# Kernel tuning notes

Measured on AMD Instinct MI355X. Metric: run time of the kernel, lower is better.

## Reference

```python
import jax, jax.numpy as jnp
import numpy as np


def setup_inputs() -> dict:
    key = jax.random.key(0)
    k1, k2 = jax.random.split(key)
    x = jax.random.normal(k1, (32, 512, 2048), dtype=jnp.float32)
    codebook = jax.random.normal(k2, (1024, 512), dtype=jnp.float32)
    return {"x": x, "codebook": codebook}


def reference(x, codebook):
    # x: [N, width, T], codebook: [nb_code, code_dim], width == code_dim
    N, width, T = x.shape
    nb_code = codebook.shape[0]
    # preprocess: [N, width, T] -> [N*T, width]
    xf = jnp.transpose(x, (0, 2, 1)).reshape(-1, width)
    dist = (jnp.sum(xf * xf, axis=-1, keepdims=True)
            - 2.0 * jnp.matmul(xf, codebook.T)
            + jnp.sum(codebook * codebook, axis=-1)[None, :])
    code_idx = jnp.argmin(dist, axis=-1)  # [N*T]
    # dequantize (embedding gather)
    x_d = codebook[code_idx]  # [N*T, width]
    # perplexity over code usage histogram
    counts = jax.ops.segment_sum(jnp.ones(code_idx.shape, dtype=x.dtype),
                                 code_idx, num_segments=nb_code)
    prob = counts / jnp.sum(counts)
    perplexity = jnp.exp(-jnp.sum(prob * jnp.log(prob + 1e-7)))
    # commitment loss against detached quantized vectors
    commit_loss = jnp.mean((xf - jax.lax.stop_gradient(x_d)) ** 2)
    # straight-through estimator
    out = xf + jax.lax.stop_gradient(x_d - xf)
    out = out.reshape(N, T, width).transpose(0, 2, 1)  # [N, width, T]
    return out, code_idx.reshape(N, T), commit_loss, perplexity
```

## Files before the change

kernel.cpp:

```cpp
#include <hip/hip_runtime.h>
#include <cstddef>
#include <cstdint>

#define N_BATCH 32
#define WIDTH   512
#define T_DIM   2048
#define NB_CODE 1024
#define M_ROWS  65536
#define OUT_ELEMS 33554432
#define IDX_OFF  OUT_ELEMS
#define LOSS_OFF (OUT_ELEMS + M_ROWS)
#define PERP_OFF (LOSS_OFF + 1)
#define MARGIN   0.75f

typedef __attribute__((ext_vector_type(8))) short vshort8;
typedef __attribute__((ext_vector_type(4))) float vfloat4;
typedef __attribute__((ext_vector_type(16))) float vfloat16;

typedef __attribute__((address_space(1))) const uint32_t gu32_t;
typedef __attribute__((address_space(3))) uint32_t lu32_t;
static __device__ __forceinline__ void gload16(const void* g, void* l) {
    __builtin_amdgcn_global_load_lds((gu32_t*)g, (lu32_t*)l, 16, 0, 0);
}

static __device__ __forceinline__ unsigned short f2bf(float f) {
    uint32_t u = __float_as_uint(f);
    uint32_t r = (u + 0x7FFFu + ((u >> 16) & 1u)) >> 16;
    return (unsigned short)r;
}


__global__ __launch_bounds__(128) void k_prep(const float* __restrict__ cb,
                                              unsigned short* __restrict__ cbh,
                                              float* __restrict__ cnorm,
                                              int* __restrict__ hist) {
    const int c = blockIdx.x, tid = threadIdx.x;
    float4 v = ((const float4*)(cb + (size_t)c * WIDTH))[tid];
    ushort4 h;
    h.x = f2bf(v.x); h.y = f2bf(v.y); h.z = f2bf(v.z); h.w = f2bf(v.w);
    ((ushort4*)(cbh + (size_t)c * WIDTH))[tid] = h;
    float s = v.x * v.x + v.y * v.y + v.z * v.z + v.w * v.w;
#pragma unroll
    for (int off = 32; off >= 1; off >>= 1) s += __shfl_xor(s, off, 64);
    __shared__ float sw[2];
    if ((tid & 63) == 0) sw[tid >> 6] = s;
    __syncthreads();
    if (tid == 0) { cnorm[c] = sw[0] + sw[1]; hist[c] = 0; }
}

__global__ __launch_bounds__(256, 2) void k_argmin(
    const float* __restrict__ x, const unsigned short* __restrict__ cbh,
    const float* __restrict__ cnorm, uint32_t* __restrict__ cand,
    float* __restrict__ sbest, float* __restrict__ xnorm) {
    __shared__ __align__(16) short lds[2][16384];

    const int tid = threadIdx.x;
    const int wv = tid >> 6, l = tid & 63;
    const int l31 = l & 31, hi = l >> 5;

    int srcoff[8];
#pragma unroll
    for (int j = 0; j < 8; ++j) {
        const int q = j * 256 + tid;
        const int code = q >> 6, w = q & 63;
        const int kb = w >> 4, s = w & 15;
        srcoff[j] = code * 1024 + kb * 256 + ((s ^ (code & 15)) << 4);
    }

#define STAGE(SP, B) do {                                                     \
    const char* cbbase_ = ((const char*)cbh) + (size_t)(SP) * 32768;          \
    short* lb_ = &lds[B][0];                                                  \
    _Pragma("unroll")                                                         \
    for (int j = 0; j < 8; ++j)                                               \
        gload16(cbbase_ + srcoff[j], lb_ + (j * 256 + tid) * 8);              \
} while (0)

    STAGE(0, 0);

    const int m0w = blockIdx.x * 128 + wv * 32;
    const int n = m0w >> 11;
    const int tcol = (m0w & 2047) + l31;
    vshort8 xh[32];
    float xn = 0.f;
    {
        const float* xb = x + (size_t)n * WIDTH * T_DIM + (size_t)hi * 8 * T_DIM + tcol;
        union U8 { uint32_t u[4]; vshort8 v; };
#pragma unroll
        for (int ks = 0; ks < 32; ++ks) {
            U8 u;
#pragma unroll
            for (int j = 0; j < 4; ++j) {
                const float f0 = xb[(size_t)(ks * 16 + 2 * j) * T_DIM];
                const float f1 = xb[(size_t)(ks * 16 + 2 * j + 1) * T_DIM];
                xn = fmaf(f0, f0, fmaf(f1, f1, xn));
                asm("v_cvt_pk_bf16_f32 %0, %1, %2" : "=v"(u.u[j]) : "v"(f0), "v"(f1));
            }
            xh[ks] = u.v;
        }
    }
    xn += __shfl_xor(xn, 32, 64);
    if (l < 32) xnorm[m0w + l] = xn;

    const int sxl = l31 & 15;
    const int rbase = l31 * 512;

    float b1 = 3.4e38f, b2 = 3.4e38f, b3 = 3.4e38f;
    int i1 = 0, i2 = 0, i3 = 0;

#define INS3(S, C) do {                                                       \
        const bool lt1 = (S) < b1, lt2 = (S) < b2, lt3 = (S) < b3;            \
        b3 = lt3 ? (lt2 ? b2 : (S)) : b3;  i3 = lt3 ? (lt2 ? i2 : (C)) : i3; \
        b2 = lt2 ? (lt1 ? b1 : (S)) : b2;  i2 = lt2 ? (lt1 ? i1 : (C)) : i2; \
        b1 = lt1 ? (S) : b1;               i1 = lt1 ? (C) : i1;              \
    } while (0)

    __syncthreads();

    for (int sp = 0; sp < 32; ++sp) {
        if (sp) {
            asm volatile("s_waitcnt vmcnt(0)" ::: "memory");
            __builtin_amdgcn_s_barrier();
        }
        if (sp < 31) {
            if (sp & 1) STAGE(sp + 1, 0); else STAGE(sp + 1, 1);
        }
        const short* buf = lds[sp & 1];
        vfloat16 acc = {};
        __builtin_amdgcn_s_setprio(1);
#pragma unroll
        for (int ks = 0; ks < 32; ++ks) {
            const int addr = rbase + (ks >> 3) * 128 +
                             (((((ks & 7) << 1) | hi) ^ sxl) << 3);
            vshort8 a = *(const vshort8*)&buf[addr];
            acc = __builtin_amdgcn_mfma_f32_32x32x16_bf16(a, xh[ks], acc, 0, 0, 0);
        }
        __builtin_amdgcn_s_setprio(0);
        const int cb0 = sp * 32;
#pragma unroll
        for (int g = 0; g < 4; ++g) {
            const int cbase = cb0 + g * 8 + 4 * hi;
            const vfloat4 cn = *(const vfloat4*)&cnorm[cbase];
#pragma unroll
            for (int j = 0; j < 4; ++j) {
                const float s = fmaf(-2.f, acc[g * 4 + j], cn[j]);
                INS3(s, cbase + j);
            }
        }
    }

    {
        const float ob1 = __shfl_xor(b1, 32, 64), ob2 = __shfl_xor(b2, 32, 64), ob3 = __shfl_xor(b3, 32, 64);
        const int oi1 = __shfl_xor(i1, 32, 64), oi2 = __shfl_xor(i2, 32, 64), oi3 = __shfl_xor(i3, 32, 64);
        INS3(ob1, oi1); INS3(ob2, oi2); INS3(ob3, oi3);
    }
    if (l < 32) {
        const uint32_t f2 = (b2 - b1 < MARGIN) ? 1u : 0u;
        const uint32_t f3 = (b3 - b1 < MARGIN) ? 1u : 0u;
        cand[m0w + l] = (uint32_t)i1 | ((uint32_t)i2 << 10) | ((uint32_t)i3 << 20) | (f2 << 30) | (f3 << 31);
        sbest[m0w + l] = b1;
    }
}

__global__ __launch_bounds__(256) void k_tail(
    const float* __restrict__ x, const float* __restrict__ cb,
    const float* __restrict__ cnorm, const uint32_t* __restrict__ cand,
    const float* __restrict__ sbest, const float* __restrict__ xnorm,
    float* __restrict__ dout, int* __restrict__ hist,
    float* __restrict__ lossPart) {
    __shared__ int sidx[64];
    __shared__ float sls[64];
    __shared__ int list[64];
    __shared__ int cnt;
    __shared__ float tile[64][130];
    const int tid = threadIdx.x;
    const int b = blockIdx.x;
    const int m0 = b * 64;
    if (tid == 0) cnt = 0;
    __syncthreads();
    if (tid < 64) {
        const uint32_t wv = cand[m0 + tid];
        sidx[tid] = (int)(wv & 1023u);
        sls[tid] = xnorm[m0 + tid] + sbest[m0 + tid];
        if (wv >> 30) { const int p = atomicAdd(&cnt, 1); list[p] = tid; }
    }
    __syncthreads();
    const int nf = cnt;
    const int w = tid >> 6, lid = tid & 63;
    for (int it = w; it < nf; it += 4) {
        const int row = m0 + list[it];
        const uint32_t wv = cand[row];
        const int j1 = (int)(wv & 1023u), j2 = (int)((wv >> 10) & 1023u), j3 = (int)((wv >> 20) & 1023u);
        const bool nd3 = (wv >> 31) & 1u;
        const int n = row >> 11, t = row & 2047;
        const float* xc = x + (size_t)n * WIDTH * T_DIM + t;
        float xv[8];
#pragma unroll
        for (int e = 0; e < 8; ++e)
            xv[e] = xc[(size_t)(lid * 8 + e) * T_DIM];
        float d1 = 0.f, d2 = 0.f, d3 = 0.f;
        {
            const float* c1 = cb + (size_t)j1 * WIDTH + lid * 8;
            const float* c2 = cb + (size_t)j2 * WIDTH + lid * 8;
            const float* c3 = cb + (size_t)j3 * WIDTH + lid * 8;
            float4 a0 = *(const float4*)c1, a1 = *(const float4*)(c1 + 4);
            d1 = fmaf(xv[0], a0.x, fmaf(xv[1], a0.y, fmaf(xv[2], a0.z, fmaf(xv[3], a0.w,
                 fmaf(xv[4], a1.x, fmaf(xv[5], a1.y, fmaf(xv[6], a1.z, xv[7] * a1.w)))))));
            float4 b0 = *(const float4*)c2, b1v = *(const float4*)(c2 + 4);
            d2 = fmaf(xv[0], b0.x, fmaf(xv[1], b0.y, fmaf(xv[2], b0.z, fmaf(xv[3], b0.w,
                 fmaf(xv[4], b1v.x, fmaf(xv[5], b1v.y, fmaf(xv[6], b1v.z, xv[7] * b1v.w)))))));
            if (nd3) {
                float4 g0 = *(const float4*)c3, g1 = *(const float4*)(c3 + 4);
                d3 = fmaf(xv[0], g0.x, fmaf(xv[1], g0.y, fmaf(xv[2], g0.z, fmaf(xv[3], g0.w,
                     fmaf(xv[4], g1.x, fmaf(xv[5], g1.y, fmaf(xv[6], g1.z, xv[7] * g1.w)))))));
            }
        }
#pragma unroll
        for (int off = 32; off >= 1; off >>= 1) {
            d1 += __shfl_xor(d1, off, 64);
            d2 += __shfl_xor(d2, off, 64);
            d3 += __shfl_xor(d3, off, 64);
        }
        if (lid == 0) {
            int win = j1;
            float qw = fmaf(-2.f, d1, cnorm[j1]);
            const float q2 = fmaf(-2.f, d2, cnorm[j2]);
            if (q2 < qw || (q2 == qw && j2 < win)) { win = j2; qw = q2; }
            if (nd3) {
                const float q3 = fmaf(-2.f, d3, cnorm[j3]);
                if (q3 < qw || (q3 == qw && j3 < win)) { win = j3; qw = q3; }
            }
            sidx[list[it]] = win;
            sls[list[it]] = xnorm[row] + qw;
        }
    }
    __syncthreads();
    if (tid < 64) {
        dout[IDX_OFF + m0 + tid] = (float)sidx[tid];
        atomicAdd(&hist[sidx[tid]], 1);
        float ls = sls[tid];
#pragma unroll
        for (int off = 32; off >= 1; off >>= 1) ls += __shfl_xor(ls, off, 64);
        if (tid == 0) lossPart[b] = ls;
    }
    const int n = b >> 5;
    const int t0 = (b & 31) * 64;
    const int l = tid & 63;
    for (int wc = 0; wc < 4; ++wc) {
#pragma unroll
        for (int rr = 0; rr < 16; ++rr) {
            const int row = w * 16 + rr;
            const float2 v = *(const float2*)(cb + (size_t)sidx[row] * WIDTH + wc * 128 + l * 2);
            *(float2*)&tile[row][l * 2] = v;
        }
        __syncthreads();
#pragma unroll 8
        for (int wwi = 0; wwi < 32; ++wwi) {
            const int ww = wc * 128 + w * 32 + wwi;
            dout[((size_t)n * WIDTH + ww) * T_DIM + t0 + l] = tile[l][w * 32 + wwi];
        }
        __syncthreads();
    }
}

__global__ __launch_bounds__(1024) void k_fin(
    const int* __restrict__ hist, const float* __restrict__ lossPart,
    float* __restrict__ dout) {
    const int tid = threadIdx.x;
    const float p = (float)hist[tid] * (1.0f / (float)M_ROWS);
    float e = p * logf(p + 1e-7f);
    float ls = lossPart[tid];
#pragma unroll
    for (int off = 32; off >= 1; off >>= 1) {
        e += __shfl_xor(e, off, 64);
        ls += __shfl_xor(ls, off, 64);
    }
    __shared__ float se[16], sl[16];
    if ((tid & 63) == 0) { se[tid >> 6] = e; sl[tid >> 6] = ls; }
    __syncthreads();
    if (tid == 0) {
        float E = 0.f, L = 0.f;
#pragma unroll
        for (int i = 0; i < 16; ++i) { E += se[i]; L += sl[i]; }
        dout[LOSS_OFF] = L / (float)OUT_ELEMS;
        dout[PERP_OFF] = expf(-E);
    }
}

extern "C" void kernel_launch(void* const* d_in, const int* in_sizes, int n_in,
                              void* d_out, int out_size, void* d_ws, size_t ws_size,
                              hipStream_t stream) {
    const float* x = (const float*)d_in[0];
    const float* cb = (const float*)d_in[1];
    float* dout = (float*)d_out;
    uint8_t* w = (uint8_t*)d_ws;

    unsigned short* cbh = (unsigned short*)w;
    float* cnorm   = (float*)(w + (1u << 20));
    int*   hist    = (int*)(w + (1u << 20) + 4096);
    uint32_t* cand = (uint32_t*)(w + (1u << 20) + 8192);
    float* sbest   = (float*)(w + (1u << 20) + 8192 + 262144);
    float* xnorm   = (float*)(w + (1u << 20) + 8192 + 2 * 262144);
    float* lossPart= (float*)(w + (1u << 20) + 8192 + 3 * 262144);

    k_prep<<<NB_CODE, 128, 0, stream>>>(cb, cbh, cnorm, hist);
    k_argmin<<<M_ROWS / 128, 256, 0, stream>>>(x, cbh, cnorm, cand, sbest, xnorm);
    k_tail<<<1024, 256, 0, stream>>>(x, cb, cnorm, cand, sbest, xnorm, dout, hist, lossPart);
    k_fin<<<1, 1024, 0, stream>>>(hist, lossPart, dout);
}
```

Baseline: 162.5 us.

## Stage codebook as 64-code by half-K tiles with two interleaved MFMA accumulators

After: 162.8 us. Within noise of the previous version (+0.2%).

```diff
diff --git a/kernel.cpp b/kernel.cpp
--- a/kernel.cpp
+++ b/kernel.cpp
@@ -62,13 +62,12 @@
 #pragma unroll
     for (int j = 0; j < 8; ++j) {
         const int q = j * 256 + tid;
-        const int code = q >> 6, w = q & 63;
-        const int kb = w >> 4, s = w & 15;
-        srcoff[j] = code * 1024 + kb * 256 + ((s ^ (code & 15)) << 4);
+        const int kq = q >> 10, code = (q >> 4) & 63, sx = q & 15;
+        srcoff[j] = code * 1024 + kq * 256 + ((sx ^ (code & 15)) << 4);
     }
 
 #define STAGE(SP, B) do {                                                     \
-    const char* cbbase_ = ((const char*)cbh) + (size_t)(SP) * 32768;          \
+    const char* cbbase_ = ((const char*)cbh) + ((SP) >> 1) * 65536 + ((SP) & 1) * 512; \
     short* lb_ = &lds[B][0];                                                  \
     _Pragma("unroll")                                                         \
     for (int j = 0; j < 8; ++j)                                               \
@@ -102,7 +101,6 @@
     if (l < 32) xnorm[m0w + l] = xn;
 
     const int sxl = l31 & 15;
-    const int rbase = l31 * 512;
 
     float b1 = 3.4e38f, b2 = 3.4e38f, b3 = 3.4e38f;
     int i1 = 0, i2 = 0, i3 = 0;
@@ -116,34 +114,44 @@
 
     __syncthreads();
 
-    for (int sp = 0; sp < 32; ++sp) {
-        if (sp) {
-            asm volatile("s_waitcnt vmcnt(0)" ::: "memory");
-            __builtin_amdgcn_s_barrier();
-        }
-        if (sp < 31) {
-            if (sp & 1) STAGE(sp + 1, 0); else STAGE(sp + 1, 1);
-        }
-        const short* buf = lds[sp & 1];
-        vfloat16 acc = {};
-        __builtin_amdgcn_s_setprio(1);
-#pragma unroll
-        for (int ks = 0; ks < 32; ++ks) {
-            const int addr = rbase + (ks >> 3) * 128 +
-                             (((((ks & 7) << 1) | hi) ^ sxl) << 3);
-            vshort8 a = *(const vshort8*)&buf[addr];
-            acc = __builtin_amdgcn_mfma_f32_32x32x16_bf16(a, xh[ks], acc, 0, 0, 0);
-        }
-        __builtin_amdgcn_s_setprio(0);
-        const int cb0 = sp * 32;
-#pragma unroll
-        for (int g = 0; g < 4; ++g) {
-            const int cbase = cb0 + g * 8 + 4 * hi;
-            const vfloat4 cn = *(const vfloat4*)&cnorm[cbase];
-#pragma unroll
-            for (int j = 0; j < 4; ++j) {
-                const float s = fmaf(-2.f, acc[g * 4 + j], cn[j]);
-                INS3(s, cbase + j);
+    for (int cc = 0; cc < 16; ++cc) {
+        vfloat16 acc0 = {}, acc1 = {};
+#pragma unroll
+        for (int kh = 0; kh < 2; ++kh) {
+            const int sp = cc * 2 + kh;
+            if (sp) {
+                asm volatile("s_waitcnt vmcnt(0)" ::: "memory");
+                __builtin_amdgcn_s_barrier();
+            }
+            if (sp < 31) {
+                if (sp & 1) STAGE(sp + 1, 0); else STAGE(sp + 1, 1);
+            }
+            const short* buf = lds[sp & 1];
+            __builtin_amdgcn_s_setprio(1);
+#pragma unroll
+            for (int ks = 0; ks < 16; ++ks) {
+                const int addr0 = (ks >> 3) * 8192 + l31 * 128 +
+                                  (((((ks & 7) << 1) | hi) ^ sxl) << 3);
+                vshort8 a0 = *(const vshort8*)&buf[addr0];
+                acc0 = __builtin_amdgcn_mfma_f32_32x32x16_bf16(a0, xh[kh * 16 + ks], acc0, 0, 0, 0);
+                vshort8 a1 = *(const vshort8*)&buf[addr0 + 4096];
+                acc1 = __builtin_amdgcn_mfma_f32_32x32x16_bf16(a1, xh[kh * 16 + ks], acc1, 0, 0, 0);
+            }
+            __builtin_amdgcn_s_setprio(0);
+        }
+        const int cb0 = cc * 64;
+#pragma unroll
+        for (int tl = 0; tl < 2; ++tl) {
+#pragma unroll
+            for (int g = 0; g < 4; ++g) {
+                const int cbase = cb0 + tl * 32 + g * 8 + 4 * hi;
+                const vfloat4 cn = *(const vfloat4*)&cnorm[cbase];
+#pragma unroll
+                for (int j = 0; j < 4; ++j) {
+                    const float a = tl ? acc1[g * 4 + j] : acc0[g * 4 + j];
+                    const float s = fmaf(-2.f, a, cn[j]);
+                    INS3(s, cbase + j);
+                }
             }
         }
     }
```
